# Kernel tuning notes

Measured on AMD Instinct MI355X. Metric: run time of the kernel, lower is better.

The kernel has to match this reference:

```python
import jax, jax.numpy as jnp
import numpy as np

# J6 incidence matrix for Plucker coordinates (constant buffer in the torch module)
_J6 = jnp.array([[0, 0, 0, 0, 0, 1],
                 [0, 0, 0, 0, -1, 0],
                 [0, 0, 0, 1, 0, 0],
                 [0, 0, 1, 0, 0, 0],
                 [0, -1, 0, 0, 0, 0],
                 [1, 0, 0, 0, 0, 0]], dtype=jnp.float32)

# combinations(range(4), 2) index pairs for the exterior product
_PI = np.array([0, 0, 0, 1, 1, 2])
_PJ = np.array([1, 2, 3, 2, 3, 3])


def plucker_lines(p1, p2):
    # p1, p2: (..., 4) -> normalized Plucker 6-vectors (..., 6)
    lines = p1[..., _PI] * p2[..., _PJ] - p1[..., _PJ] * p2[..., _PI]
    n = jnp.linalg.norm(lines, axis=-1, keepdims=True)
    return lines / jnp.maximum(n, 1e-12)


def setup_inputs() -> dict:
    key = jax.random.key(0)
    ks = jax.random.split(key, 6)
    B, T, D, H = 1, 2048, 1024, 16
    s = D ** -0.5
    x = jax.random.normal(ks[0], (B, T, D), jnp.float32)
    Wqkv = jax.random.normal(ks[1], (D, 3 * D), jnp.float32) * s
    bqkv = jnp.zeros((3 * D,), jnp.float32)
    W1p = jax.random.normal(ks[2], (D, 4 * H), jnp.float32) * s
    W2p = jax.random.normal(ks[3], (D, 4 * H), jnp.float32) * s
    plucker_scale = jnp.full((H,), 0.1, jnp.float32)
    Wout = jax.random.normal(ks[4], (D, D), jnp.float32) * s
    bout = jnp.zeros((D,), jnp.float32)
    return {"x": x, "Wqkv": Wqkv, "bqkv": bqkv, "W1p": W1p, "W2p": W2p,
            "plucker_scale": plucker_scale, "Wout": Wout, "bout": bout}


def reference(x, Wqkv, bqkv, W1p, W2p, plucker_scale, Wout, bout):
    B, T, D = x.shape
    H = plucker_scale.shape[0]
    dh = D // H

    qkv = (x @ Wqkv + bqkv).reshape(B, T, 3, H, dh)
    q = jnp.transpose(qkv[:, :, 0], (0, 2, 1, 3))  # [B,H,T,dh]
    k = jnp.transpose(qkv[:, :, 1], (0, 2, 1, 3))
    v = jnp.transpose(qkv[:, :, 2], (0, 2, 1, 3))

    std_logits = jnp.einsum('bhid,bhjd->bhij', q, k) * (dh ** -0.5)

    p1 = (x @ W1p).reshape(B, T, H, 4)
    p2 = (x @ W2p).reshape(B, T, H, 4)
    lines_h = jnp.transpose(plucker_lines(p1, p2), (0, 2, 1, 3))  # [B,H,T,6]
    Jlines = lines_h @ _J6.T                                       # [B,H,T,6]
    plucker_bias = jnp.einsum('bhic,bhjc->bhij', lines_h, Jlines)  # [B,H,T,T]

    logits = std_logits + plucker_bias * plucker_scale[None, :, None, None]
    causal = jnp.triu(jnp.ones((T, T), bool), 1)
    logits = jnp.where(causal[None, None], -jnp.inf, logits)
    attn = jax.nn.softmax(logits, axis=-1)

    out = jnp.einsum('bhij,bhjd->bhid', attn, v)
    out = jnp.transpose(out, (0, 2, 1, 3)).reshape(B, T, D)
    return out @ Wout + bout
```

## Files before the change

kernel.cpp:

```cpp
#include <hip/hip_runtime.h>

typedef unsigned short u16;
typedef unsigned int u32;
typedef __attribute__((ext_vector_type(8))) __bf16 bf16x8;
typedef __attribute__((ext_vector_type(4))) float f32x4;
typedef __attribute__((ext_vector_type(4))) u16 u16x4;

#define MFMA16(a, b, c) __builtin_amdgcn_mfma_f32_16x16x32_bf16((a), (b), (c), 0, 0, 0)

static __device__ __forceinline__ u16 f2b(float f) {
  union { float f; u32 u; } v; v.f = f;
  u32 u = v.u;
  return (u16)((u + 0x7FFFu + ((u >> 16) & 1u)) >> 16);
}

static __device__ __forceinline__ u32 pack2(float a, float b) {
  u32 r;
  asm("v_cvt_pk_bf16_f32 %0, %1, %2" : "=v"(r) : "v"(a), "v"(b));
  return r;
}

static __device__ __forceinline__ float exp2fast(float x) {
#if defined(__has_builtin) && __has_builtin(__builtin_amdgcn_exp2f)
  return __builtin_amdgcn_exp2f(x);
#else
  return __expf(x * 0.6931471805599453f);
#endif
}

static __device__ __forceinline__ void gload16(const u16* gp, u16* lp) {
  __builtin_amdgcn_global_load_lds((__attribute__((address_space(1))) void*)(u16*)gp,
                                   (__attribute__((address_space(3))) void*)lp, 16, 0, 0);
}

__global__ __launch_bounds__(256) void k_prep(const float* __restrict__ Wqkv, const float* __restrict__ Wout,
                                              const float* __restrict__ W1p, const float* __restrict__ W2p,
                                              const float* __restrict__ x,
                                              u16* __restrict__ WB, u16* __restrict__ WoT,
                                              u16* __restrict__ xb) {
  const int b = blockIdx.x;
  const int t = threadIdx.x;
  if (b < 4096) {
    __shared__ float tile[32][33];
    const float* src; u16* dst; int N, n0, k0;
    if (b < 3072) { src = Wqkv; dst = WB;  N = 3072; n0 = (b % 96) * 32; k0 = (b / 96) * 32; }
    else { const int bb = b - 3072; src = Wout; dst = WoT; N = 1024; n0 = (bb & 31) * 32; k0 = (bb >> 5) * 32; }
    const int r = t >> 3, c4 = (t & 7) << 2;
    const float4 in4 = *(const float4*)(src + (size_t)(k0 + r) * N + n0 + c4);
    tile[r][c4 + 0] = in4.x; tile[r][c4 + 1] = in4.y;
    tile[r][c4 + 2] = in4.z; tile[r][c4 + 3] = in4.w;
    __syncthreads();
    u16x4 o;
    o.x = f2b(tile[c4 + 0][r]); o.y = f2b(tile[c4 + 1][r]);
    o.z = f2b(tile[c4 + 2][r]); o.w = f2b(tile[c4 + 3][r]);
    *(u16x4*)(dst + (size_t)(n0 + r) * 1024 + k0 + c4) = o;
  } else if (b < 4608) {
    const int idx = (b - 4096) * 256 + t;
    const int j = idx >> 10, k = idx & 1023;
    const float v = (j < 64) ? W1p[(size_t)k * 64 + j] : W2p[(size_t)k * 64 + (j - 64)];
    WB[(size_t)3072 * 1024 + idx] = f2b(v);
  } else {
    const size_t idx = ((size_t)(b - 4608) * 256 + t) << 2;
    const float4 v = *(const float4*)(x + idx);
    u16x4 o; o.x = f2b(v.x); o.y = f2b(v.y); o.z = f2b(v.z); o.w = f2b(v.w);
    *(u16x4*)(xb + idx) = o;
  }
}

static __device__ __forceinline__ void gemm_core_128x64(const u16* __restrict__ A, const u16* __restrict__ B,
                                                        int brow, int bcol, int K,
                                                        u16* ldsA, u16* ldsB, f32x4 acc[4][2]) {
  const int tid = threadIdx.x;
  const int wave = tid >> 6, lane = tid & 63;
  const int wr = wave >> 1, wc = wave & 1;
  const int g = lane >> 4, l15 = lane & 15;

  for (int k0 = 0; k0 < K; k0 += 64) {
#pragma unroll
    for (int li = 0; li < 4; ++li) {
      const int f = li * 256 + wave * 64 + lane;
      const int row = f >> 3;
      const int slot = f & 7;
      const int gcol = ((slot ^ (row & 7)) << 3);
      gload16(A + (size_t)(brow + row) * K + k0 + gcol, ldsA + (size_t)(li * 256 + wave * 64) * 8);
    }
#pragma unroll
    for (int li = 0; li < 2; ++li) {
      const int f = li * 256 + wave * 64 + lane;
      const int row = f >> 3;
      const int slot = f & 7;
      const int gcol = ((slot ^ (row & 7)) << 3);
      gload16(B + (size_t)(bcol + row) * K + k0 + gcol, ldsB + (size_t)(li * 256 + wave * 64) * 8);
    }
    __syncthreads();
    bf16x8 af[4][2], bfr[2][2];
#pragma unroll
    for (int kk = 0; kk < 2; ++kk) {
#pragma unroll
      for (int m = 0; m < 4; ++m) {
        const int rowA = wr * 64 + m * 16 + l15;
        const int chA = (kk * 4 + g) ^ (rowA & 7);
        af[m][kk] = *(const bf16x8*)(ldsA + (size_t)rowA * 64 + chA * 8);
      }
#pragma unroll
      for (int n = 0; n < 2; ++n) {
        const int rowB = wc * 32 + n * 16 + l15;
        const int chB = (kk * 4 + g) ^ (rowB & 7);
        bfr[n][kk] = *(const bf16x8*)(ldsB + (size_t)rowB * 64 + chB * 8);
      }
    }
#pragma unroll
    for (int m = 0; m < 4; ++m)
#pragma unroll
      for (int n = 0; n < 2; ++n)
#pragma unroll
        for (int kk = 0; kk < 2; ++kk)
          acc[m][n] = MFMA16(af[m][kk], bfr[n][kk], acc[m][n]);
    __syncthreads();
  }
}

__global__ __launch_bounds__(256) void k_gemm_qkvp(const u16* __restrict__ xb, const u16* __restrict__ WB,
                                                   const float* __restrict__ bqkv,
                                                   u16* __restrict__ Qext, u16* __restrict__ Kext,
                                                   u16* __restrict__ Vt, float* __restrict__ P12) {
  __shared__ __align__(16) u16 ldsA[128 * 64];
  __shared__ __align__(16) u16 ldsB[64 * 64];
  const int bid = blockIdx.x;
  const int bn = bid % 50, bm = bid / 50;
  f32x4 acc[4][2];
#pragma unroll
  for (int m = 0; m < 4; ++m)
#pragma unroll
    for (int n = 0; n < 2; ++n) acc[m][n] = (f32x4){0.f, 0.f, 0.f, 0.f};
  gemm_core_128x64(xb, WB, bm * 128, bn * 64, 1024, ldsA, ldsB, acc);

  const int tid = threadIdx.x;
  const int wave = tid >> 6, lane = tid & 63;
  const int wr = wave >> 1, wc = wave & 1;
  const int g = lane >> 4, l15 = lane & 15;
  const int tbase = bm * 128 + wr * 64 + g * 4;
  const int cbase = bn * 64 + wc * 32 + l15;
#pragma unroll
  for (int m = 0; m < 4; ++m) {
#pragma unroll
    for (int n = 0; n < 2; ++n) {
      const int c = cbase + n * 16;
#pragma unroll
      for (int r = 0; r < 4; ++r) {
        const int t = tbase + m * 16 + r;
        float v = acc[m][n][r];
        if (c < 3072) {
          v += bqkv[c];
          const int sub = c >> 10;
          const int rem = c & 1023;
          const int hh = rem >> 6, d = rem & 63;
          if (sub == 0)      Qext[((size_t)hh * 2048 + t) * 96 + d] = f2b(v * 0.18033688f);
          else if (sub == 1) Kext[((size_t)hh * 2048 + t) * 96 + d] = f2b(v);
          else               Vt[((size_t)hh * 64 + d) * 2048 + t] = f2b(v);
        } else {
          P12[(size_t)t * 128 + (c - 3072)] = v;
        }
      }
    }
  }
}

__global__ __launch_bounds__(256) void k_lines(const float* __restrict__ P12, const float* __restrict__ pscale,
                                               u16* __restrict__ Qext, u16* __restrict__ Kext) {
  const int idx = blockIdx.x * 256 + threadIdx.x;
  const int t = idx >> 4, h = idx & 15;
  const float* p = P12 + (size_t)t * 128;
  const float a0 = p[h * 4 + 0], a1 = p[h * 4 + 1], a2 = p[h * 4 + 2], a3 = p[h * 4 + 3];
  const float b0 = p[64 + h * 4 + 0], b1 = p[64 + h * 4 + 1], b2 = p[64 + h * 4 + 2], b3 = p[64 + h * 4 + 3];
  float L0 = a0 * b1 - a1 * b0;
  float L1 = a0 * b2 - a2 * b0;
  float L2 = a0 * b3 - a3 * b0;
  float L3 = a1 * b2 - a2 * b1;
  float L4 = a1 * b3 - a3 * b1;
  float L5 = a2 * b3 - a3 * b2;
  const float nrm = sqrtf(L0 * L0 + L1 * L1 + L2 * L2 + L3 * L3 + L4 * L4 + L5 * L5);
  const float inv = 1.0f / fmaxf(nrm, 1e-12f);
  L0 *= inv; L1 *= inv; L2 *= inv; L3 *= inv; L4 *= inv; L5 *= inv;
  const float s = pscale[h] * 1.44269504f;
  u16* q = Qext + ((size_t)h * 2048 + t) * 96 + 64;
  u16* k = Kext + ((size_t)h * 2048 + t) * 96 + 64;
  q[0] = f2b(L0 * s); q[1] = f2b(L1 * s); q[2] = f2b(L2 * s);
  q[3] = f2b(L3 * s); q[4] = f2b(L4 * s); q[5] = f2b(L5 * s);
  k[0] = f2b(L5); k[1] = f2b(-L4); k[2] = f2b(L3);
  k[3] = f2b(L2); k[4] = f2b(-L1); k[5] = f2b(L0);
#pragma unroll
  for (int c = 6; c < 32; ++c) { q[c] = 0; k[c] = 0; }
}

__global__ __launch_bounds__(64) void k_attn(const u16* __restrict__ Qext, const u16* __restrict__ Kext,
                                             const u16* __restrict__ Vt, u16* __restrict__ AO) {
  const int bid = blockIdx.x;
  const int h = bid & 15;
  const int p = bid >> 4;
  const int lane = threadIdx.x;
  const int g = lane >> 4, l15 = lane & 15;
  const int q0A = p << 4;
  const int q0B = (127 - p) << 4;
  const int qgA = q0A + l15;
  const int qgB = q0B + l15;
  const int sA = (p >> 1) + 1;
  const int sB = ((127 - p) >> 1) + 1;
  const u16* Qh = Qext + (size_t)h * 2048 * 96;
  const u16* Kh = Kext + (size_t)h * 2048 * 96;
  const u16* Vh = Vt + (size_t)h * 64 * 2048;

  bf16x8 aqA[3], aqB[3];
#pragma unroll
  for (int ks = 0; ks < 3; ++ks) {
    aqA[ks] = *(const bf16x8*)(Qh + (size_t)qgA * 96 + ks * 32 + g * 8);
    aqB[ks] = *(const bf16x8*)(Qh + (size_t)qgB * 96 + ks * 32 + g * 8);
  }

  f32x4 accA[4], accB[4];
#pragma unroll
  for (int n = 0; n < 4; ++n) {
    accA[n] = (f32x4){0.f, 0.f, 0.f, 0.f};
    accB[n] = (f32x4){0.f, 0.f, 0.f, 0.f};
  }
  float lA = 0.f, lB = 0.f;

  const u16* Kbase = Kh + (size_t)l15 * 96 + g * 8;
  const int src0 = ((g & 1) << 5) + l15;
  const int src1 = src0 + 16;

  bf16x8 kX0[3], kX1[3], kY0[3], kY1[3];
#pragma unroll
  for (int ks = 0; ks < 3; ++ks) {
    kX0[ks] = *(const bf16x8*)(Kbase + ks * 32);
    kX1[ks] = *(const bf16x8*)(Kbase + 16 * 96 + ks * 32);
  }

#define GLUE(S0, S1, Q0S, QGS, LS, PBS)                                           \
  {                                                                               \
    if (jb + 31 > Q0S) {                                                          \
      _Pragma("unroll")                                                           \
      for (int r = 0; r < 4; ++r) {                                               \
        if (jb + g * 4 + r > QGS) S0[r] = -1e30f;                                 \
        if (jb + 16 + g * 4 + r > QGS) S1[r] = -1e30f;                            \
      }                                                                           \
    }                                                                             \
    _Pragma("unroll")                                                             \
    for (int r = 0; r < 4; ++r) {                                                 \
      S0[r] = exp2fast(S0[r]);                                                    \
      S1[r] = exp2fast(S1[r]);                                                    \
    }                                                                             \
    LS += ((S0[0] + S0[1]) + (S0[2] + S0[3])) + ((S1[0] + S1[1]) + (S1[2] + S1[3])); \
    const u32 w0 = pack2(S0[0], S0[1]);                                           \
    const u32 w1 = pack2(S0[2], S0[3]);                                           \
    const u32 w2 = pack2(S1[0], S1[1]);                                           \
    const u32 w3 = pack2(S1[2], S1[3]);                                           \
    const u32 a0 = (u32)__shfl((int)w0, src0);                                    \
    const u32 a1 = (u32)__shfl((int)w2, src0);                                    \
    const u32 b0 = (u32)__shfl((int)w1, src0);                                    \
    const u32 b1 = (u32)__shfl((int)w3, src0);                                    \
    const u32 c0 = (u32)__shfl((int)w0, src1);                                    \
    const u32 c1 = (u32)__shfl((int)w2, src1);                                    \
    const u32 d0 = (u32)__shfl((int)w1, src1);                                    \
    const u32 d1 = (u32)__shfl((int)w3, src1);                                    \
    PBS.u[0] = (g & 2) ? a1 : a0;                                                 \
    PBS.u[1] = (g & 2) ? b1 : b0;                                                 \
    PBS.u[2] = (g & 2) ? c1 : c0;                                                 \
    PBS.u[3] = (g & 2) ? d1 : d0;                                                 \
  }

#define ATTN_STEP(KC0, KC1, KN0, KN1)                                             \
  {                                                                               \
    const int jb = jt * 32;                                                       \
    const bool actA = (jt < sA);                                                  \
    f32x4 SB0 = (f32x4){0.f, 0.f, 0.f, 0.f}, SB1 = (f32x4){0.f, 0.f, 0.f, 0.f};   \
    f32x4 SA0 = (f32x4){0.f, 0.f, 0.f, 0.f}, SA1 = (f32x4){0.f, 0.f, 0.f, 0.f};   \
    __builtin_amdgcn_s_setprio(1);                                                \
    _Pragma("unroll")                                                             \
    for (int ks = 0; ks < 3; ++ks) {                                              \
      SB0 = MFMA16(KC0[ks], aqB[ks], SB0);                                        \
      SB1 = MFMA16(KC1[ks], aqB[ks], SB1);                                        \
    }                                                                             \
    if (actA) {                                                                   \
      _Pragma("unroll")                                                           \
      for (int ks = 0; ks < 3; ++ks) {                                            \
        SA0 = MFMA16(KC0[ks], aqA[ks], SA0);                                      \
        SA1 = MFMA16(KC1[ks], aqA[ks], SA1);                                      \
      }                                                                           \
    }                                                                             \
    __builtin_amdgcn_s_setprio(0);                                                \
    bf16x8 av[4];                                                   \
    _Pragma("unroll")                                                             \
    for (int n = 0; n < 4; ++n)                                                   \
      av[n] = *(const bf16x8*)(Vh + (size_t)(n * 16 + l15) * 2048 + jb + g * 8);  \
    const int jbn = (jt + 1 < sB) ? jb + 32 : jb;          \
    const u16* kp = Kbase + (size_t)jbn * 96;                                     \
    _Pragma("unroll")                                                             \
    for (int ks = 0; ks < 3; ++ks) {                                              \
      KN0[ks] = *(const bf16x8*)(kp + ks * 32);                                   \
      KN1[ks] = *(const bf16x8*)(kp + 16 * 96 + ks * 32);                         \
    }                                                                             \
    union { u32 u[4]; bf16x8 bv; } pbB, pbA;                                      \
    GLUE(SB0, SB1, q0B, qgB, lB, pbB);                                            \
    if (actA) GLUE(SA0, SA1, q0A, qgA, lA, pbA);                                  \
    __builtin_amdgcn_s_setprio(1);                                                \
    _Pragma("unroll")                                                             \
    for (int n = 0; n < 4; ++n) accB[n] = MFMA16(av[n], pbB.bv, accB[n]);         \
    if (actA) {                                                                   \
      _Pragma("unroll")                                                           \
      for (int n = 0; n < 4; ++n) accA[n] = MFMA16(av[n], pbA.bv, accA[n]);       \
    }                                                                             \
    __builtin_amdgcn_s_setprio(0);                                                \
  }

  int jt = 0;
  for (;;) {
    ATTN_STEP(kX0, kX1, kY0, kY1);
    if (++jt >= sB) break;
    ATTN_STEP(kY0, kY1, kX0, kX1);
    if (++jt >= sB) break;
  }
#undef ATTN_STEP
#undef GLUE

  lA += __shfl_xor(lA, 16);
  lA += __shfl_xor(lA, 32);
  lB += __shfl_xor(lB, 16);
  lB += __shfl_xor(lB, 32);
  const float invA = 1.0f / lA;
  const float invB = 1.0f / lB;
  u32* dstA = (u32*)(AO + (size_t)qgA * 1024 + h * 64 + g * 4);
  u32* dstB = (u32*)(AO + (size_t)qgB * 1024 + h * 64 + g * 4);
#pragma unroll
  for (int n = 0; n < 4; ++n) {
    dstA[n * 8 + 0] = pack2(accA[n][0] * invA, accA[n][1] * invA);
    dstA[n * 8 + 1] = pack2(accA[n][2] * invA, accA[n][3] * invA);
    dstB[n * 8 + 0] = pack2(accB[n][0] * invB, accB[n][1] * invB);
    dstB[n * 8 + 1] = pack2(accB[n][2] * invB, accB[n][3] * invB);
  }
}

__global__ __launch_bounds__(256) void k_gemm_out(const u16* __restrict__ AO, const u16* __restrict__ WoT,
                                                  const float* __restrict__ bout, float* __restrict__ out) {
  __shared__ __align__(16) u16 ldsA[128 * 64];
  __shared__ __align__(16) u16 ldsB[64 * 64];
  const int bid = blockIdx.x;
  const int bn = bid & 15, bm = bid >> 4;
  f32x4 acc[4][2];
#pragma unroll
  for (int m = 0; m < 4; ++m)
#pragma unroll
    for (int n = 0; n < 2; ++n) acc[m][n] = (f32x4){0.f, 0.f, 0.f, 0.f};
  gemm_core_128x64(AO, WoT, bm * 128, bn * 64, 1024, ldsA, ldsB, acc);

  const int tid = threadIdx.x;
  const int wave = tid >> 6, lane = tid & 63;
  const int wr = wave >> 1, wc = wave & 1;
  const int g = lane >> 4, l15 = lane & 15;
  const int tbase = bm * 128 + wr * 64 + g * 4;
  const int cbase = bn * 64 + wc * 32 + l15;
#pragma unroll
  for (int m = 0; m < 4; ++m)
#pragma unroll
    for (int n = 0; n < 2; ++n) {
      const int c = cbase + n * 16;
      const float bb = bout[c];
#pragma unroll
      for (int r = 0; r < 4; ++r) {
        const int t = tbase + m * 16 + r;
        out[(size_t)t * 1024 + c] = acc[m][n][r] + bb;
      }
    }
}

extern "C" void kernel_launch(void* const* d_in, const int* in_sizes, int n_in,
                              void* d_out, int out_size, void* d_ws, size_t ws_size,
                              hipStream_t stream) {
  const float* x      = (const float*)d_in[0];
  const float* Wqkv   = (const float*)d_in[1];
  const float* bqkv   = (const float*)d_in[2];
  const float* W1p    = (const float*)d_in[3];
  const float* W2p    = (const float*)d_in[4];
  const float* pscale = (const float*)d_in[5];
  const float* Wout   = (const float*)d_in[6];
  const float* bout   = (const float*)d_in[7];
  float* out = (float*)d_out;

  char* ws = (char*)d_ws;
  u16*   WB    = (u16*)(ws + 0);
  u16*   WoT   = (u16*)(ws + 6553600);
  u16*   xb    = (u16*)(ws + 8650752);
  u16*   Qext  = (u16*)(ws + 12845056);
  u16*   Kext  = (u16*)(ws + 19136512);
  u16*   Vt    = (u16*)(ws + 25427968);
  float* P12   = (float*)(ws + 29622272);
  u16*   AO    = (u16*)(ws + 30670848);

  k_prep<<<6656, 256, 0, stream>>>(Wqkv, Wout, W1p, W2p, x, WB, WoT, xb);
  k_gemm_qkvp<<<800, 256, 0, stream>>>(xb, WB, bqkv, Qext, Kext, Vt, P12);
  k_lines<<<128, 256, 0, stream>>>(P12, pscale, Qext, Kext);
  k_attn<<<1024, 64, 0, stream>>>(Qext, Kext, Vt, AO);
  k_gemm_out<<<256, 256, 0, stream>>>(AO, WoT, bout, out);
}
```

Measured before the change: 111.1 us.

## Split attention key range across two blocks and add a combine kernel

The causal attention kernel now splits each query pair's key-tile range in half across two blocks, doubling the grid from 1024 to 2048 single-wave blocks. Each block writes its unnormalized partial output (bf16) and row sums to scratch. A new combine kernel adds the partials, normalizes and writes AO in the layout the output GEMM expects. This targets low occupancy and long per-block serial loops. It costs an extra launch, extra scratch traffic and some precision from storing unnormalized partials in bf16. The split only runs when the workspace is large enough.

```diff
diff --git a/kernel.cpp b/kernel.cpp
--- a/kernel.cpp
+++ b/kernel.cpp
@@ -12,6 +12,10 @@
   union { float f; u32 u; } v; v.f = f;
   u32 u = v.u;
   return (u16)((u + 0x7FFFu + ((u >> 16) & 1u)) >> 16);
+}
+
+static __device__ __forceinline__ float b2f(u16 s) {
+  union { u32 u; float f; } c; c.u = (u32)s << 16; return c.f;
 }
 
 static __device__ __forceinline__ u32 pack2(float a, float b) {
@@ -194,10 +198,14 @@
 }
 
 __global__ __launch_bounds__(64) void k_attn(const u16* __restrict__ Qext, const u16* __restrict__ Kext,
-                                             const u16* __restrict__ Vt, u16* __restrict__ AO) {
+                                             const u16* __restrict__ Vt,
+                                             u16* __restrict__ Op0, u16* __restrict__ Op1,
+                                             float* __restrict__ lp0, float* __restrict__ lp1,
+                                             int nsplit) {
   const int bid = blockIdx.x;
+  const int split = bid >> 10;
   const int h = bid & 15;
-  const int p = bid >> 4;
+  const int p = (bid >> 4) & 63;
   const int lane = threadIdx.x;
   const int g = lane >> 4, l15 = lane & 15;
   const int q0A = p << 4;
@@ -206,6 +214,9 @@
   const int qgB = q0B + l15;
   const int sA = (p >> 1) + 1;
   const int sB = ((127 - p) >> 1) + 1;
+  const int mid = sB >> 1;
+  const int jBeg = (nsplit == 2 && split) ? mid : 0;
+  const int jEnd = (nsplit == 2 && !split) ? mid : sB;
   const u16* Qh = Qext + (size_t)h * 2048 * 96;
   const u16* Kh = Kext + (size_t)h * 2048 * 96;
   const u16* Vh = Vt + (size_t)h * 64 * 2048;
@@ -230,11 +241,6 @@
   const int src1 = src0 + 16;
 
   bf16x8 kX0[3], kX1[3], kY0[3], kY1[3];
-#pragma unroll
-  for (int ks = 0; ks < 3; ++ks) {
-    kX0[ks] = *(const bf16x8*)(Kbase + ks * 32);
-    kX1[ks] = *(const bf16x8*)(Kbase + 16 * 96 + ks * 32);
-  }
 
 #define GLUE(S0, S1, Q0S, QGS, LS, PBS)                                           \
   {                                                                               \
@@ -293,7 +299,7 @@
     _Pragma("unroll")                                                             \
     for (int n = 0; n < 4; ++n)                                                   \
       av[n] = *(const bf16x8*)(Vh + (size_t)(n * 16 + l15) * 2048 + jb + g * 8);  \
-    const int jbn = (jt + 1 < sB) ? jb + 32 : jb;          \
+    const int jbn = (jt + 1 < jEnd) ? jb + 32 : jb;        \
     const u16* kp = Kbase + (size_t)jbn * 96;                                     \
     _Pragma("unroll")                                                             \
     for (int ks = 0; ks < 3; ++ks) {                                              \
@@ -313,12 +319,20 @@
     __builtin_amdgcn_s_setprio(0);                                                \
   }
 
-  int jt = 0;
-  for (;;) {
-    ATTN_STEP(kX0, kX1, kY0, kY1);
-    if (++jt >= sB) break;
-    ATTN_STEP(kY0, kY1, kX0, kX1);
-    if (++jt >= sB) break;
+  int jt = jBeg;
+  {
+    const u16* kp0 = Kbase + (size_t)jt * 32 * 96;
+#pragma unroll
+    for (int ks = 0; ks < 3; ++ks) {
+      kX0[ks] = *(const bf16x8*)(kp0 + ks * 32);
+      kX1[ks] = *(const bf16x8*)(kp0 + 16 * 96 + ks * 32);
+    }
+    for (;;) {
+      ATTN_STEP(kX0, kX1, kY0, kY1);
+      if (++jt >= jEnd) break;
+      ATTN_STEP(kY0, kY1, kX0, kX1);
+      if (++jt >= jEnd) break;
+    }
   }
 #undef ATTN_STEP
 #undef GLUE
@@ -327,17 +341,53 @@
   lA += __shfl_xor(lA, 32);
   lB += __shfl_xor(lB, 16);
   lB += __shfl_xor(lB, 32);
-  const float invA = 1.0f / lA;
-  const float invB = 1.0f / lB;
-  u32* dstA = (u32*)(AO + (size_t)qgA * 1024 + h * 64 + g * 4);
-  u32* dstB = (u32*)(AO + (size_t)qgB * 1024 + h * 64 + g * 4);
+  u16* Op = split ? Op1 : Op0;
+  float* lp = split ? lp1 : lp0;
+  const size_t sbA = ((size_t)h * 2048 + qgA) * 64 + g * 4;
+  const size_t sbB = ((size_t)h * 2048 + qgB) * 64 + g * 4;
 #pragma unroll
   for (int n = 0; n < 4; ++n) {
-    dstA[n * 8 + 0] = pack2(accA[n][0] * invA, accA[n][1] * invA);
-    dstA[n * 8 + 1] = pack2(accA[n][2] * invA, accA[n][3] * invA);
-    dstB[n * 8 + 0] = pack2(accB[n][0] * invB, accB[n][1] * invB);
-    dstB[n * 8 + 1] = pack2(accB[n][2] * invB, accB[n][3] * invB);
-  }
+    uint2 wa, wb;
+    wa.x = pack2(accA[n][0], accA[n][1]);
+    wa.y = pack2(accA[n][2], accA[n][3]);
+    wb.x = pack2(accB[n][0], accB[n][1]);
+    wb.y = pack2(accB[n][2], accB[n][3]);
+    *(uint2*)(Op + sbA + n * 16) = wa;
+    *(uint2*)(Op + sbB + n * 16) = wb;
+  }
+  if (lane < 16) {
+    lp[(size_t)h * 2048 + qgA] = lA;
+    lp[(size_t)h * 2048 + qgB] = lB;
+  }
+}
+
+__global__ __launch_bounds__(256) void k_comb(const u16* __restrict__ Op0, const u16* __restrict__ Op1,
+                                              const float* __restrict__ lp0, const float* __restrict__ lp1,
+                                              u16* __restrict__ AO, int nsplit) {
+  const int idx = blockIdx.x * 256 + threadIdx.x;
+  const int d8 = idx & 7;
+  const int hq = idx >> 3;
+  const int q = hq & 2047, h = hq >> 11;
+  float l = lp0[hq];
+  union { uint4 v; u16 s[8]; } a;
+  a.v = *(const uint4*)(Op0 + (size_t)hq * 64 + d8 * 8);
+  float o[8];
+#pragma unroll
+  for (int i = 0; i < 8; ++i) o[i] = b2f(a.s[i]);
+  if (nsplit == 2) {
+    l += lp1[hq];
+    union { uint4 v; u16 s[8]; } bb;
+    bb.v = *(const uint4*)(Op1 + (size_t)hq * 64 + d8 * 8);
+#pragma unroll
+    for (int i = 0; i < 8; ++i) o[i] += b2f(bb.s[i]);
+  }
+  const float inv = 1.0f / l;
+  uint4 w;
+  w.x = pack2(o[0] * inv, o[1] * inv);
+  w.y = pack2(o[2] * inv, o[3] * inv);
+  w.z = pack2(o[4] * inv, o[5] * inv);
+  w.w = pack2(o[6] * inv, o[7] * inv);
+  *(uint4*)(AO + (size_t)q * 1024 + h * 64 + d8 * 8) = w;
 }
 
 __global__ __launch_bounds__(256) void k_gemm_out(const u16* __restrict__ AO, const u16* __restrict__ WoT,
@@ -396,9 +446,17 @@
   float* P12   = (float*)(ws + 29622272);
   u16*   AO    = (u16*)(ws + 30670848);
 
+  u16*   Op0   = xb;
+  float* lp0   = P12;
+  u16*   Op1   = (u16*)(ws + 34865152);
+  float* lp1   = (float*)(ws + 39059456);
+  const int nsplit = (ws_size >= 39190528ull) ? 2 : 1;
+  if (nsplit == 1) { Op1 = Op0; lp1 = lp0; }
+
   k_prep<<<6656, 256, 0, stream>>>(Wqkv, Wout, W1p, W2p, x, WB, WoT, xb);
   k_gemm_qkvp<<<800, 256, 0, stream>>>(xb, WB, bqkv, Qext, Kext, Vt, P12);
   k_lines<<<128, 256, 0, stream>>>(P12, pscale, Qext, Kext);
-  k_attn<<<1024, 64, 0, stream>>>(Qext, Kext, Vt, AO);
+  k_attn<<<1024 * nsplit, 64, 0, stream>>>(Qext, Kext, Vt, Op0, Op1, lp0, lp1, nsplit);
+  k_comb<<<1024, 256, 0, stream>>>(Op0, Op1, lp0, lp1, AO, nsplit);
   k_gemm_out<<<256, 256, 0, stream>>>(AO, WoT, bout, out);
 }
```

After: 117.9 us. 1.06x slower.

## Use 128x128 tiles for QKV projection GEMM and block V layout per 32 keys

Applied to the files above, without the earlier changes.

Adds a 128x128 GEMM core so the fused QKV/Plucker projection runs 400 blocks instead of 800, each with a larger output tile. This doubles operand reuse out of LDS per loaded tile. V is now stored in 32-key blocks ([h][t/32][d][32]), so each attention iteration reads a contiguous 4KB chunk instead of rows 4KB apart. The trade-offs are more accumulator registers and LDS per block, and fewer blocks to cover the CUs.

```diff
diff --git a/kernel.cpp b/kernel.cpp
--- a/kernel.cpp
+++ b/kernel.cpp
@@ -67,6 +67,53 @@
   }
 }
 
+static __device__ __forceinline__ void gemm128_core(const u16* __restrict__ A, const u16* __restrict__ B,
+                                                    int brow, int bcol, int K,
+                                                    u16* ldsA, u16* ldsB, f32x4 acc[4][4]) {
+  const int tid = threadIdx.x;
+  const int wave = tid >> 6, lane = tid & 63;
+  const int wr = wave >> 1, wc = wave & 1;
+  const int g = lane >> 4, l15 = lane & 15;
+
+  for (int k0 = 0; k0 < K; k0 += 64) {
+#pragma unroll
+    for (int li = 0; li < 4; ++li) {
+      const int f = li * 256 + wave * 64 + lane;
+      const int row = f >> 3;
+      const int slot = f & 7;
+      const int gcol = ((slot ^ (row & 7)) << 3);
+      const u16* ga = A + (size_t)(brow + row) * K + k0 + gcol;
+      const u16* gb = B + (size_t)(bcol + row) * K + k0 + gcol;
+      u16* la = ldsA + (size_t)(li * 256 + wave * 64) * 8;
+      u16* lb = ldsB + (size_t)(li * 256 + wave * 64) * 8;
+      gload16(ga, la);
+      gload16(gb, lb);
+    }
+    __syncthreads();
+    bf16x8 af[4][2], bfr[4][2];
+#pragma unroll
+    for (int m = 0; m < 4; ++m) {
+#pragma unroll
+      for (int kk = 0; kk < 2; ++kk) {
+        const int rowA = wr * 64 + m * 16 + l15;
+        const int chA = (kk * 4 + g) ^ (rowA & 7);
+        af[m][kk] = *(const bf16x8*)(ldsA + (size_t)rowA * 64 + chA * 8);
+        const int rowB = wc * 64 + m * 16 + l15;
+        const int chB = (kk * 4 + g) ^ (rowB & 7);
+        bfr[m][kk] = *(const bf16x8*)(ldsB + (size_t)rowB * 64 + chB * 8);
+      }
+    }
+#pragma unroll
+    for (int m = 0; m < 4; ++m)
+#pragma unroll
+      for (int n = 0; n < 4; ++n)
+#pragma unroll
+        for (int kk = 0; kk < 2; ++kk)
+          acc[m][n] = MFMA16(af[m][kk], bfr[n][kk], acc[m][n]);
+    __syncthreads();
+  }
+}
+
 static __device__ __forceinline__ void gemm_core_128x64(const u16* __restrict__ A, const u16* __restrict__ B,
                                                         int brow, int bcol, int K,
                                                         u16* ldsA, u16* ldsB, f32x4 acc[4][2]) {
@@ -125,26 +172,26 @@
                                                    u16* __restrict__ Qext, u16* __restrict__ Kext,
                                                    u16* __restrict__ Vt, float* __restrict__ P12) {
   __shared__ __align__(16) u16 ldsA[128 * 64];
-  __shared__ __align__(16) u16 ldsB[64 * 64];
+  __shared__ __align__(16) u16 ldsB[128 * 64];
   const int bid = blockIdx.x;
-  const int bn = bid % 50, bm = bid / 50;
-  f32x4 acc[4][2];
+  const int bn = bid % 25, bm = bid / 25;
+  f32x4 acc[4][4];
 #pragma unroll
   for (int m = 0; m < 4; ++m)
 #pragma unroll
-    for (int n = 0; n < 2; ++n) acc[m][n] = (f32x4){0.f, 0.f, 0.f, 0.f};
-  gemm_core_128x64(xb, WB, bm * 128, bn * 64, 1024, ldsA, ldsB, acc);
+    for (int n = 0; n < 4; ++n) acc[m][n] = (f32x4){0.f, 0.f, 0.f, 0.f};
+  gemm128_core(xb, WB, bm * 128, bn * 128, 1024, ldsA, ldsB, acc);
 
   const int tid = threadIdx.x;
   const int wave = tid >> 6, lane = tid & 63;
   const int wr = wave >> 1, wc = wave & 1;
   const int g = lane >> 4, l15 = lane & 15;
   const int tbase = bm * 128 + wr * 64 + g * 4;
-  const int cbase = bn * 64 + wc * 32 + l15;
+  const int cbase = bn * 128 + wc * 64 + l15;
 #pragma unroll
   for (int m = 0; m < 4; ++m) {
 #pragma unroll
-    for (int n = 0; n < 2; ++n) {
+    for (int n = 0; n < 4; ++n) {
       const int c = cbase + n * 16;
 #pragma unroll
       for (int r = 0; r < 4; ++r) {
@@ -157,7 +204,7 @@
           const int hh = rem >> 6, d = rem & 63;
           if (sub == 0)      Qext[((size_t)hh * 2048 + t) * 96 + d] = f2b(v * 0.18033688f);
           else if (sub == 1) Kext[((size_t)hh * 2048 + t) * 96 + d] = f2b(v);
-          else               Vt[((size_t)hh * 64 + d) * 2048 + t] = f2b(v);
+          else               Vt[(size_t)hh * 131072 + (size_t)(t >> 5) * 2048 + d * 32 + (t & 31)] = f2b(v);
         } else {
           P12[(size_t)t * 128 + (c - 3072)] = v;
         }
@@ -208,7 +255,7 @@
   const int sB = ((127 - p) >> 1) + 1;
   const u16* Qh = Qext + (size_t)h * 2048 * 96;
   const u16* Kh = Kext + (size_t)h * 2048 * 96;
-  const u16* Vh = Vt + (size_t)h * 64 * 2048;
+  const u16* Vh = Vt + (size_t)h * 131072;
 
   bf16x8 aqA[3], aqB[3];
 #pragma unroll
@@ -289,10 +336,10 @@
       }                                                                           \
     }                                                                             \
     __builtin_amdgcn_s_setprio(0);                                                \
-    bf16x8 av[4];                                                   \
+    bf16x8 av[4];            \
     _Pragma("unroll")                                                             \
     for (int n = 0; n < 4; ++n)                                                   \
-      av[n] = *(const bf16x8*)(Vh + (size_t)(n * 16 + l15) * 2048 + jb + g * 8);  \
+      av[n] = *(const bf16x8*)(Vh + (size_t)jb * 64 + (n * 16 + l15) * 32 + g * 8); \
     const int jbn = (jt + 1 < sB) ? jb + 32 : jb;          \
     const u16* kp = Kbase + (size_t)jbn * 96;                                     \
     _Pragma("unroll")                                                             \
@@ -397,7 +444,7 @@
   u16*   AO    = (u16*)(ws + 30670848);
 
   k_prep<<<6656, 256, 0, stream>>>(Wqkv, Wout, W1p, W2p, x, WB, WoT, xb);
-  k_gemm_qkvp<<<800, 256, 0, stream>>>(xb, WB, bqkv, Qext, Kext, Vt, P12);
+  k_gemm_qkvp<<<400, 256, 0, stream>>>(xb, WB, bqkv, Qext, Kext, Vt, P12);
   k_lines<<<128, 256, 0, stream>>>(P12, pscale, Qext, Kext);
   k_attn<<<1024, 64, 0, stream>>>(Qext, Kext, Vt, AO);
   k_gemm_out<<<256, 256, 0, stream>>>(AO, WoT, bout, out);
```

After: 113.1 us. About the same (+1.8%).
